# Optimization experiments

Hardware: AMD Instinct MI355X
Metric: run time of the kernel (lower is better)

Reference implementation:

```python
import jax, jax.numpy as jnp
import numpy as np

D = 64       # desc_dim
PD = 64      # pose_dim
NH = 4       # num_heads
PS = 5       # patch_size
B, N, H, W = 16, 1024, 256, 256


def setup_inputs() -> dict:
    key = jax.random.key(0)
    ks = jax.random.split(key, 16)
    s = 1.0 / np.sqrt(D)
    inp = {
        "desc_points": jax.random.normal(ks[0], (B, N, D), jnp.float32),
        "shared_feat_map": jax.random.normal(ks[1], (B, D, H, W), jnp.float32),
        "coords": jax.random.randint(ks[2], (B, N, 2), 0, H),
        "pose_embed": jax.random.normal(ks[3], (B, PD), jnp.float32),
        "Wq": jax.random.normal(ks[4], (D, D), jnp.float32) * s,
        "bq": jnp.zeros((D,), jnp.float32),
        "Wk": jax.random.normal(ks[5], (D, D), jnp.float32) * s,
        "bk": jnp.zeros((D,), jnp.float32),
        "Wv": jax.random.normal(ks[6], (D, D), jnp.float32) * s,
        "bv": jnp.zeros((D,), jnp.float32),
        "Wp": jax.random.normal(ks[7], (PD, D), jnp.float32) * s,
        "bp": jnp.zeros((D,), jnp.float32),
        "Wo": jax.random.normal(ks[8], (D, D), jnp.float32) * s,
        "bo": jnp.zeros((D,), jnp.float32),
    }
    return inp


def _patch_means(feat_map, coords):
    # feat_map: [B,C,H,W], coords: [B,N,2] int (y,x). Vectorized ROI mean-pool.
    pad = PS // 2
    padded = jnp.pad(feat_map, ((0, 0), (0, 0), (pad, pad), (pad, pad)))
    y = coords[..., 0]
    x = coords[..., 1]
    off = jnp.arange(PS)
    rows = y[:, :, None, None] + off[None, None, :, None]   # [B,N,PS,1]
    cols = x[:, :, None, None] + off[None, None, None, :]   # [B,N,1,PS]
    bidx = jnp.arange(feat_map.shape[0])[:, None, None, None]
    # advanced indexing: result [B,N,PS,PS,C]
    patches = padded[bidx, :, rows, cols]
    return patches.mean(axis=(2, 3))  # [B,N,C]


def reference(desc_points, shared_feat_map, coords, pose_embed,
              Wq, bq, Wk, bk, Wv, bv, Wp, bp, Wo, bo):
    b, n, c = desc_points.shape
    hd = c // NH
    patch_feats = _patch_means(shared_feat_map, coords)  # [B,N,C]

    q = (desc_points @ Wq + bq).reshape(b, n, NH, hd)
    k = (patch_feats @ Wk + bk).reshape(b, n, NH, hd)
    v = (patch_feats @ Wv + bv).reshape(b, n, NH, hd)

    scores = jnp.einsum('bnhd,bmhd->bhnm', q, k) / jnp.sqrt(jnp.float32(hd))
    probs = jax.nn.softmax(scores, axis=-1)
    attn = jnp.einsum('bhnm,bmhd->bnhd', probs, v).reshape(b, n, c)

    pose_mod = pose_embed @ Wp + bp               # [B,C]
    fused = attn * (1.0 + pose_mod[:, None, :])   # [B,N,C]
    return fused @ Wo + bo
```

## Files before the change

kernel.cpp:

```cpp
#include <hip/hip_runtime.h>
#include <hip/hip_bf16.h>
#include <cstdint>
#include <cstddef>

#define BB 16
#define NN 1024
#define DD 64
#define NHH 4
#define HDD 16
#define KSPL 8

#define OFF_Q  0
#define OFF_K  (OFF_Q + BB*NHH*NN*HDD)
#define OFF_V  (OFF_K + BB*NHH*NN*HDD)
#define OFF_L  (OFF_V + BB*NHH*NN*HDD)
#define OFF_AT (OFF_L + KSPL*64*NN)
#define OFF_PM (OFF_AT + (size_t)KSPL*64*NN*HDD)
#define OFF_TP (OFF_PM + 1024)
#define NEED_FULL  ((size_t)(OFF_TP + (size_t)BB*256*256*DD) * 4)

__global__ __launch_bounds__(256) void k_tpose2(
    const float* __restrict__ fm, float* __restrict__ TP)
{
    int t   = threadIdx.x;
    int pxl = t >> 2, cq = t & 3;
    int bid = blockIdx.x;
    int b   = bid >> 10;
    int pb  = bid & 1023;
    size_t pxg = (size_t)pb * 64 + pxl;

    const float* src = fm + ((size_t)b << 22);
    float*       dst = TP + ((size_t)b << 22) + pxg * 64;

    float4 vals[4];
    #pragma unroll
    for (int j = 0; j < 4; ++j) {
        int c0 = (cq + 4 * j) * 4;
        vals[j].x = src[((size_t)(c0 + 0) << 16) + pxg];
        vals[j].y = src[((size_t)(c0 + 1) << 16) + pxg];
        vals[j].z = src[((size_t)(c0 + 2) << 16) + pxg];
        vals[j].w = src[((size_t)(c0 + 3) << 16) + pxg];
    }
    #pragma unroll
    for (int j = 0; j < 4; ++j)
        *(float4*)(dst + (cq + 4 * j) * 4) = vals[j];
}

__global__ __launch_bounds__(256) void k_pf_qkv4(
    const float* __restrict__ desc, const float* __restrict__ TP,
    const int* __restrict__ coords,
    const float* __restrict__ Wq, const float* __restrict__ bq,
    const float* __restrict__ Wk, const float* __restrict__ bk,
    const float* __restrict__ Wv, const float* __restrict__ bv,
    float* __restrict__ Q, float* __restrict__ K, float* __restrict__ V)
{
    int w   = threadIdx.x >> 6;
    int c   = threadIdx.x & 63;
    int pid = blockIdx.x * 4 + w;
    int b   = pid >> 10;
    int n   = pid & 1023;

    __shared__ float spf[4][64];
    __shared__ float sd[4][64];

    int y = coords[pid * 2 + 0];
    int x = coords[pid * 2 + 1];

    const float* tp = TP + ((size_t)b << 22) + c;
    float s = 0.f;
    #pragma unroll
    for (int dy = -2; dy <= 2; ++dy) {
        int yy = y + dy;
        if ((unsigned)yy < 256u) {
            const float* rp = tp + ((size_t)yy << 14);
            #pragma unroll
            for (int dx = -2; dx <= 2; ++dx) {
                int xx = x + dx;
                if ((unsigned)xx < 256u) s += rp[(size_t)xx << 6];
            }
        }
    }
    spf[w][c] = s * 0.04f;
    sd[w][c]  = desc[(size_t)pid * 64 + c];
    __syncthreads();

    float aq = bq[c], ak = bk[c], av = bv[c];
    #pragma unroll 8
    for (int i = 0; i < 64; ++i) {
        float xd = sd[w][i];
        float xp = spf[w][i];
        aq = fmaf(xd, Wq[i * 64 + c], aq);
        ak = fmaf(xp, Wk[i * 64 + c], ak);
        av = fmaf(xp, Wv[i * 64 + c], av);
    }
    int h = c >> 4, d = c & 15;
    size_t o = (((size_t)b * 4 + h) * 1024 + n) * 16 + d;
    Q[o] = aq; K[o] = ak; V[o] = av;
}

__global__ __launch_bounds__(256) void k_pf_qkv(
    const float* __restrict__ desc, const float* __restrict__ fm,
    const int* __restrict__ coords,
    const float* __restrict__ Wq, const float* __restrict__ bq,
    const float* __restrict__ Wk, const float* __restrict__ bk,
    const float* __restrict__ Wv, const float* __restrict__ bv,
    float* __restrict__ Q, float* __restrict__ K, float* __restrict__ V)
{
    int w   = threadIdx.x >> 6;
    int c   = threadIdx.x & 63;
    int pid = blockIdx.x * 4 + w;
    int b   = pid >> 10;
    int n   = pid & 1023;

    __shared__ float spf[4][64];
    __shared__ float sd[4][64];

    int y = coords[pid * 2 + 0];
    int x = coords[pid * 2 + 1];

    const float* fmc = fm + ((size_t)(b * 64 + c) << 16);
    float s = 0.f;
    #pragma unroll
    for (int dy = -2; dy <= 2; ++dy) {
        int yy = y + dy;
        if ((unsigned)yy < 256u) {
            const float* row = fmc + yy * 256;
            #pragma unroll
            for (int dx = -2; dx <= 2; ++dx) {
                int xx = x + dx;
                if ((unsigned)xx < 256u) s += row[xx];
            }
        }
    }
    spf[w][c] = s * 0.04f;
    sd[w][c]  = desc[(size_t)pid * 64 + c];
    __syncthreads();

    float aq = bq[c], ak = bk[c], av = bv[c];
    #pragma unroll 8
    for (int i = 0; i < 64; ++i) {
        float xd = sd[w][i];
        float xp = spf[w][i];
        aq = fmaf(xd, Wq[i * 64 + c], aq);
        ak = fmaf(xp, Wk[i * 64 + c], ak);
        av = fmaf(xp, Wv[i * 64 + c], av);
    }
    int h = c >> 4, d = c & 15;
    size_t o = (((size_t)b * 4 + h) * 1024 + n) * 16 + d;
    Q[o] = aq; K[o] = ak; V[o] = av;
}

__global__ __launch_bounds__(64) void k_pose(
    const float* __restrict__ pe, const float* __restrict__ Wp,
    const float* __restrict__ bp, float* __restrict__ pm1)
{
    int b = blockIdx.x, c = threadIdx.x;
    __shared__ float sp[64];
    sp[c] = pe[b * 64 + c];
    __syncthreads();
    float acc = bp[c];
    #pragma unroll 8
    for (int i = 0; i < 64; ++i) acc = fmaf(sp[i], Wp[i * 64 + c], acc);
    pm1[b * 64 + c] = 1.f + acc;
}

__global__ __launch_bounds__(256, 2) void k_attn3(
    const float* __restrict__ Q, const float* __restrict__ K,
    const float* __restrict__ V,
    float* __restrict__ lpart, float* __restrict__ apart)
{
    int s  = blockIdx.x & 7;
    int bh = blockIdx.x >> 3;
    int t  = threadIdx.x;

    const float4* Kb = ((const float4*)K) + ((size_t)bh << 12) + ((size_t)s << 9);
    const float4* Vb = ((const float4*)V) + ((size_t)bh << 12) + ((size_t)s << 9);

    float4 q[4][4];
    float4 A[4][4];
    float  l[4];
    #pragma unroll
    for (int i = 0; i < 4; ++i) {
        const float4* qp = ((const float4*)Q) + (((size_t)bh << 10) + t + 256 * i) * 4;
        #pragma unroll
        for (int j = 0; j < 4; ++j) { q[i][j] = qp[j]; A[i][j] = make_float4(0.f,0.f,0.f,0.f); }
        l[i] = 0.f;
    }

    for (int m = 0; m < 128; ++m) {
        float4 ka = Kb[m*4+0], kb = Kb[m*4+1], kc = Kb[m*4+2], kd = Kb[m*4+3];
        float4 va = Vb[m*4+0], vb = Vb[m*4+1], vc = Vb[m*4+2], vd = Vb[m*4+3];
        #pragma unroll
        for (int i = 0; i < 4; ++i) {
            float sc = q[i][0].x*ka.x + q[i][0].y*ka.y + q[i][0].z*ka.z + q[i][0].w*ka.w
                     + q[i][1].x*kb.x + q[i][1].y*kb.y + q[i][1].z*kb.z + q[i][1].w*kb.w
                     + q[i][2].x*kc.x + q[i][2].y*kc.y + q[i][2].z*kc.z + q[i][2].w*kc.w
                     + q[i][3].x*kd.x + q[i][3].y*kd.y + q[i][3].z*kd.z + q[i][3].w*kd.w;
            float p = __expf(sc * 0.25f);
            l[i] += p;
            A[i][0].x = fmaf(p, va.x, A[i][0].x); A[i][0].y = fmaf(p, va.y, A[i][0].y);
            A[i][0].z = fmaf(p, va.z, A[i][0].z); A[i][0].w = fmaf(p, va.w, A[i][0].w);
            A[i][1].x = fmaf(p, vb.x, A[i][1].x); A[i][1].y = fmaf(p, vb.y, A[i][1].y);
            A[i][1].z = fmaf(p, vb.z, A[i][1].z); A[i][1].w = fmaf(p, vb.w, A[i][1].w);
            A[i][2].x = fmaf(p, vc.x, A[i][2].x); A[i][2].y = fmaf(p, vc.y, A[i][2].y);
            A[i][2].z = fmaf(p, vc.z, A[i][2].z); A[i][2].w = fmaf(p, vc.w, A[i][2].w);
            A[i][3].x = fmaf(p, vd.x, A[i][3].x); A[i][3].y = fmaf(p, vd.y, A[i][3].y);
            A[i][3].z = fmaf(p, vd.z, A[i][3].z); A[i][3].w = fmaf(p, vd.w, A[i][3].w);
        }
    }

    #pragma unroll
    for (int i = 0; i < 4; ++i) {
        size_t ro = (size_t)(s * 64 + bh) * 1024 + (t + 256 * i);
        lpart[ro] = l[i];
        float4* ap = (float4*)apart + ro * 4;
        ap[0] = A[i][0]; ap[1] = A[i][1]; ap[2] = A[i][2]; ap[3] = A[i][3];
    }
}

__global__ __launch_bounds__(256) void k_out(
    const float* __restrict__ lpart, const float* __restrict__ apart,
    const float* __restrict__ pm1, const float* __restrict__ Wo,
    const float* __restrict__ bo, float* __restrict__ out)
{
    int w   = threadIdx.x >> 6;
    int c   = threadIdx.x & 63;
    int pid = blockIdx.x * 4 + w;
    int b   = pid >> 10;
    int n   = pid & 1023;
    int h   = c >> 4, d = c & 15;
    int bh  = b * 4 + h;

    __shared__ float sf[4][64];

    float a = 0.f, ls = 0.f;
    #pragma unroll
    for (int s = 0; s < KSPL; ++s) {
        size_t ro = (size_t)(s * 64 + bh) * 1024 + n;
        a  += apart[(ro << 4) + d];
        ls += lpart[ro];
    }
    sf[w][c] = (a / ls) * pm1[b * 64 + c];
    __syncthreads();

    float acc = bo[c];
    #pragma unroll 8
    for (int i = 0; i < 64; ++i) acc = fmaf(sf[w][i], Wo[i * 64 + c], acc);
    out[(size_t)pid * 64 + c] = acc;
}

extern "C" void kernel_launch(void* const* d_in, const int* in_sizes, int n_in,
                              void* d_out, int out_size, void* d_ws, size_t ws_size,
                              hipStream_t stream)
{
    const float* desc = (const float*)d_in[0];
    const float* fm   = (const float*)d_in[1];
    const int*   crd  = (const int*)  d_in[2];
    const float* pe   = (const float*)d_in[3];
    const float* Wq   = (const float*)d_in[4];
    const float* bq   = (const float*)d_in[5];
    const float* Wk   = (const float*)d_in[6];
    const float* bk   = (const float*)d_in[7];
    const float* Wv   = (const float*)d_in[8];
    const float* bv   = (const float*)d_in[9];
    const float* Wp   = (const float*)d_in[10];
    const float* bp   = (const float*)d_in[11];
    const float* Wo   = (const float*)d_in[12];
    const float* bo   = (const float*)d_in[13];
    float* out = (float*)d_out;

    float* ws    = (float*)d_ws;
    float* Qb    = ws + OFF_Q;
    float* Kb    = ws + OFF_K;
    float* Vb    = ws + OFF_V;
    float* lpart = ws + OFF_L;
    float* apart = ws + OFF_AT;
    float* pm1   = ws + OFF_PM;
    float* TP    = ws + OFF_TP;

    if (ws_size >= NEED_FULL) {
        hipLaunchKernelGGL(k_tpose2, dim3(BB * 1024), dim3(256), 0, stream, fm, TP);
        hipLaunchKernelGGL(k_pf_qkv4, dim3(BB * NN / 4), dim3(256), 0, stream,
                           desc, TP, crd, Wq, bq, Wk, bk, Wv, bv, Qb, Kb, Vb);
    } else {
        hipLaunchKernelGGL(k_pf_qkv, dim3(BB * NN / 4), dim3(256), 0, stream,
                           desc, fm, crd, Wq, bq, Wk, bk, Wv, bv, Qb, Kb, Vb);
    }
    hipLaunchKernelGGL(k_pose, dim3(BB), dim3(64), 0, stream, pe, Wp, bp, pm1);
    hipLaunchKernelGGL(k_attn3, dim3(64 * KSPL), dim3(256), 0, stream,
                       Qb, Kb, Vb, lpart, apart);
    hipLaunchKernelGGL(k_out, dim3(BB * NN / 4), dim3(256), 0, stream,
                       lpart, apart, pm1, Wo, bo, out);
}
```

Baseline: 601.3 us.

## Fuse horizontal 5-tap box sum into transpose pass; gather only vertical taps

The channel-last transpose kernel is replaced by one that reads a row of the feature map with coalesced float4 loads, computes a horizontal 5-wide box sum with wave shuffles, and writes the transposed result through LDS. The patch-mean gather then needs only 5 vertical loads per channel instead of 25. This cuts random gather traffic and makes the transpose read coalesced, at the cost of extra shuffles and LDS use in the transpose. The full-size intermediate buffer is still written and read.

```diff
diff --git a/kernel.cpp b/kernel.cpp
--- a/kernel.cpp
+++ b/kernel.cpp
@@ -1,5 +1,4 @@
 #include <hip/hip_runtime.h>
-#include <hip/hip_bf16.h>
 #include <cstdint>
 #include <cstddef>
 
@@ -19,35 +18,58 @@
 #define OFF_TP (OFF_PM + 1024)
 #define NEED_FULL  ((size_t)(OFF_TP + (size_t)BB*256*256*DD) * 4)
 
-__global__ __launch_bounds__(256) void k_tpose2(
-    const float* __restrict__ fm, float* __restrict__ TP)
-{
+#define SL 260
+
+__global__ __launch_bounds__(256) void k_thsum(
+    const float* __restrict__ fm, float* __restrict__ HS)
+{
+    __shared__ float L[32 * SL];
     int t   = threadIdx.x;
-    int pxl = t >> 2, cq = t & 3;
     int bid = blockIdx.x;
-    int b   = bid >> 10;
-    int pb  = bid & 1023;
-    size_t pxg = (size_t)pb * 64 + pxl;
-
-    const float* src = fm + ((size_t)b << 22);
-    float*       dst = TP + ((size_t)b << 22) + pxg * 64;
-
-    float4 vals[4];
-    #pragma unroll
-    for (int j = 0; j < 4; ++j) {
-        int c0 = (cq + 4 * j) * 4;
-        vals[j].x = src[((size_t)(c0 + 0) << 16) + pxg];
-        vals[j].y = src[((size_t)(c0 + 1) << 16) + pxg];
-        vals[j].z = src[((size_t)(c0 + 2) << 16) + pxg];
-        vals[j].w = src[((size_t)(c0 + 3) << 16) + pxg];
-    }
-    #pragma unroll
-    for (int j = 0; j < 4; ++j)
-        *(float4*)(dst + (cq + 4 * j) * 4) = vals[j];
-}
-
-__global__ __launch_bounds__(256) void k_pf_qkv4(
-    const float* __restrict__ desc, const float* __restrict__ TP,
+    int b   = bid >> 9;
+    int y   = (bid >> 1) & 255;
+    int ch  = bid & 1;
+
+    int w = t >> 6, l = t & 63;
+    const float* src = fm + ((size_t)b << 22) + ((size_t)(ch * 32) << 16) + ((size_t)y << 8);
+    #pragma unroll
+    for (int i = 0; i < 8; ++i) {
+        int c = w * 8 + i;
+        float4 v = *(const float4*)(src + ((size_t)c << 16) + l * 4);
+        float pz = __shfl_up(v.z, 1);
+        float pw = __shfl_up(v.w, 1);
+        float nx = __shfl_down(v.x, 1);
+        float ny = __shfl_down(v.y, 1);
+        if (l == 0)  { pz = 0.f; pw = 0.f; }
+        if (l == 63) { nx = 0.f; ny = 0.f; }
+        float s3 = v.x + v.y + v.z;
+        float s4 = s3 + v.w;
+        float4 hs;
+        hs.x = pz + pw + s3;
+        hs.y = pw + s4;
+        hs.z = s4 + nx;
+        hs.w = v.y + v.z + v.w + nx + ny;
+        *(float4*)(&L[c * SL + 4 * l]) = hs;
+    }
+    __syncthreads();
+
+    int k   = t & 7;
+    int pxw = t >> 3;
+    float* dst = HS + ((size_t)b << 22) + ((size_t)y << 14) + ch * 32;
+    #pragma unroll
+    for (int i = 0; i < 8; ++i) {
+        int px = i * 32 + pxw;
+        float4 o;
+        o.x = L[(4 * k + 0) * SL + px];
+        o.y = L[(4 * k + 1) * SL + px];
+        o.z = L[(4 * k + 2) * SL + px];
+        o.w = L[(4 * k + 3) * SL + px];
+        *(float4*)(dst + (size_t)px * 64 + 4 * k) = o;
+    }
+}
+
+__global__ __launch_bounds__(256) void k_pf_qkv5(
+    const float* __restrict__ desc, const float* __restrict__ HS,
     const int* __restrict__ coords,
     const float* __restrict__ Wq, const float* __restrict__ bq,
     const float* __restrict__ Wk, const float* __restrict__ bk,
@@ -66,19 +88,12 @@
     int y = coords[pid * 2 + 0];
     int x = coords[pid * 2 + 1];
 
-    const float* tp = TP + ((size_t)b << 22) + c;
+    const float* hp = HS + ((size_t)b << 22) + ((size_t)x << 6) + c;
     float s = 0.f;
     #pragma unroll
     for (int dy = -2; dy <= 2; ++dy) {
         int yy = y + dy;
-        if ((unsigned)yy < 256u) {
-            const float* rp = tp + ((size_t)yy << 14);
-            #pragma unroll
-            for (int dx = -2; dx <= 2; ++dx) {
-                int xx = x + dx;
-                if ((unsigned)xx < 256u) s += rp[(size_t)xx << 6];
-            }
-        }
+        if ((unsigned)yy < 256u) s += hp[(size_t)yy << 14];
     }
     spf[w][c] = s * 0.04f;
     sd[w][c]  = desc[(size_t)pid * 64 + c];
@@ -276,12 +291,12 @@
     float* lpart = ws + OFF_L;
     float* apart = ws + OFF_AT;
     float* pm1   = ws + OFF_PM;
-    float* TP    = ws + OFF_TP;
+    float* HS    = ws + OFF_TP;
 
     if (ws_size >= NEED_FULL) {
-        hipLaunchKernelGGL(k_tpose2, dim3(BB * 1024), dim3(256), 0, stream, fm, TP);
-        hipLaunchKernelGGL(k_pf_qkv4, dim3(BB * NN / 4), dim3(256), 0, stream,
-                           desc, TP, crd, Wq, bq, Wk, bk, Wv, bv, Qb, Kb, Vb);
+        hipLaunchKernelGGL(k_thsum, dim3(BB * 256 * 2), dim3(256), 0, stream, fm, HS);
+        hipLaunchKernelGGL(k_pf_qkv5, dim3(BB * NN / 4), dim3(256), 0, stream,
+                           desc, HS, crd, Wq, bq, Wk, bk, Wv, bv, Qb, Kb, Vb);
     } else {
         hipLaunchKernelGGL(k_pf_qkv, dim3(BB * NN / 4), dim3(256), 0, stream,
                            desc, fm, crd, Wq, bq, Wk, bk, Wv, bv, Qb, Kb, Vb);
```

Result: faster. 568.9 us (-5.4%).
